# Optimization experiments

Measured on AMD Instinct MI355X. Metric: run time of the kernel, lower is better.

## Reference

```python
import jax, jax.numpy as jnp
import numpy as np

N, D = 8192, 1024
MAX_REP = 8

def setup_inputs() -> dict:
    key = jax.random.key(0)
    k1, k2 = jax.random.split(key)
    encoder_h = jax.random.normal(k1, (N, D), dtype=jnp.float32)
    repeats = jax.random.randint(k2, (N,), 0, MAX_REP, dtype=jnp.int32)
    return {"encoder_h": encoder_h, "repeats": repeats}

def reference(encoder_h, repeats):
    # Variable-length repeat_interleave along axis 0.
    # Equivalent to tf tile+sequence_mask+boolean_mask+reshape in the original,
    # but expressed as a single cumsum-index gather (no max_repeat-sized blowup).
    repeats = repeats.astype(jnp.int32)
    total = int(jnp.sum(repeats))  # dynamic output length (data-dependent)
    csum = jnp.cumsum(repeats)                     # [N]
    # row index for each output slot: searchsorted maps output position -> source row
    idx = jnp.searchsorted(csum, jnp.arange(total, dtype=jnp.int32), side='right')  # [total]
    return encoder_h[idx]                          # [total, D]
```

## Files before the change

### kernel.cpp

```cpp
#include <hip/hip_runtime.h>


#define SCAN_THREADS 1024
#define ELEMS_PER_THREAD 8

__global__ __launch_bounds__(SCAN_THREADS)
void scan_kernel(const int* __restrict__ repeats, int* __restrict__ csum, int n) {
    __shared__ int tmp[SCAN_THREADS];
    const int t = threadIdx.x;
    const int base = t * ELEMS_PER_THREAD;
    int vals[ELEMS_PER_THREAD];
    int s = 0;
#pragma unroll
    for (int j = 0; j < ELEMS_PER_THREAD; ++j) {
        const int idx = base + j;
        const int v = (idx < n) ? repeats[idx] : 0;
        vals[j] = v;
        s += v;
    }
    tmp[t] = s;
    __syncthreads();
    for (int off = 1; off < SCAN_THREADS; off <<= 1) {
        const int v = (t >= off) ? tmp[t - off] : 0;
        __syncthreads();
        tmp[t] += v;
        __syncthreads();
    }
    int run = tmp[t] - s;
#pragma unroll
    for (int j = 0; j < ELEMS_PER_THREAD; ++j) {
        run += vals[j];
        const int idx = base + j;
        if (idx < n) csum[idx] = run;
    }
}

__global__ __launch_bounds__(256)
void gather_rows_kernel(const float* __restrict__ h,
                        const int* __restrict__ csum,
                        float* __restrict__ out,
                        int n_rows_in, int d4 ) {
    const int row = blockIdx.x;
    int lo = 0, hi = n_rows_in;
    while (lo < hi) {
        const int mid = (lo + hi) >> 1;
        if (csum[mid] > row) hi = mid; else lo = mid + 1;
    }
    const float4* __restrict__ src = (const float4*)h + (size_t)lo * d4;
    float4* __restrict__ dst = (float4*)out + (size_t)row * d4;
    for (int i = threadIdx.x; i < d4; i += blockDim.x) {
        dst[i] = src[i];
    }
}

extern "C" void kernel_launch(void* const* d_in, const int* in_sizes, int n_in,
                              void* d_out, int out_size, void* d_ws, size_t ws_size,
                              hipStream_t stream) {
    const float* encoder_h = (const float*)d_in[0];
    const int*   repeats   = (const int*)d_in[1];
    float*       out       = (float*)d_out;

    const int n = in_sizes[1];
    const int d = in_sizes[0] / n;
    const int total_rows = out_size / d;

    int* csum = (int*)d_ws;

    scan_kernel<<<1, SCAN_THREADS, 0, stream>>>(repeats, csum, n);
    gather_rows_kernel<<<total_rows, 256, 0, stream>>>(encoder_h, csum, out,
                                                       n, d / 4);
}
```

Measured before the change: 170.6 us.

## Scatter explicit row index map in scan kernel; gather multiple rows per block

The scan kernel now writes each output row's source index directly into a workspace map, replacing the per-block binary search over the cumulative sum in the gather kernel. The gather kernel also handles four output rows per block, loading their indices up front. This removes about thirteen dependent global reads per output row before the copy starts and cuts block count. In exchange the single-block scan does serial scattered writes whose length varies per thread, and the workspace must hold total_rows ints instead of n.

```diff
diff --git a/kernel.cpp b/kernel.cpp
--- a/kernel.cpp
+++ b/kernel.cpp
@@ -3,9 +3,11 @@
 
 #define SCAN_THREADS 1024
 #define ELEMS_PER_THREAD 8
+#define ROWS_PER_BLOCK 4
 
 __global__ __launch_bounds__(SCAN_THREADS)
-void scan_kernel(const int* __restrict__ repeats, int* __restrict__ csum, int n) {
+void scan_scatter_kernel(const int* __restrict__ repeats,
+                         int* __restrict__ idx_map, int n) {
     __shared__ int tmp[SCAN_THREADS];
     const int t = threadIdx.x;
     const int base = t * ELEMS_PER_THREAD;
@@ -29,27 +31,36 @@
     int run = tmp[t] - s;
 #pragma unroll
     for (int j = 0; j < ELEMS_PER_THREAD; ++j) {
-        run += vals[j];
-        const int idx = base + j;
-        if (idx < n) csum[idx] = run;
+        const int src_row = base + j;
+        const int r = vals[j];
+        for (int k = 0; k < r; ++k) {
+            idx_map[run + k] = src_row;
+        }
+        run += r;
     }
 }
 
 __global__ __launch_bounds__(256)
-void gather_rows_kernel(const float* __restrict__ h,
-                        const int* __restrict__ csum,
-                        float* __restrict__ out,
-                        int n_rows_in, int d4 ) {
-    const int row = blockIdx.x;
-    int lo = 0, hi = n_rows_in;
-    while (lo < hi) {
-        const int mid = (lo + hi) >> 1;
-        if (csum[mid] > row) hi = mid; else lo = mid + 1;
+void gather_rows_kernel(const float4* __restrict__ h,
+                        const int* __restrict__ idx_map,
+                        float4* __restrict__ out,
+                        int total_rows, int d4 ) {
+    const int row0 = blockIdx.x * ROWS_PER_BLOCK;
+    int srcs[ROWS_PER_BLOCK];
+#pragma unroll
+    for (int r = 0; r < ROWS_PER_BLOCK; ++r) {
+        const int row = row0 + r;
+        srcs[r] = (row < total_rows) ? idx_map[row] : 0;
     }
-    const float4* __restrict__ src = (const float4*)h + (size_t)lo * d4;
-    float4* __restrict__ dst = (float4*)out + (size_t)row * d4;
-    for (int i = threadIdx.x; i < d4; i += blockDim.x) {
-        dst[i] = src[i];
+#pragma unroll
+    for (int r = 0; r < ROWS_PER_BLOCK; ++r) {
+        const int row = row0 + r;
+        if (row >= total_rows) return;
+        const float4* __restrict__ src = h + (size_t)srcs[r] * d4;
+        float4* __restrict__ dst = out + (size_t)row * d4;
+        for (int i = threadIdx.x; i < d4; i += blockDim.x) {
+            dst[i] = src[i];
+        }
     }
 }
 
@@ -64,9 +75,11 @@
     const int d = in_sizes[0] / n;
     const int total_rows = out_size / d;
 
-    int* csum = (int*)d_ws;
+    int* idx_map = (int*)d_ws;
 
-    scan_kernel<<<1, SCAN_THREADS, 0, stream>>>(repeats, csum, n);
-    gather_rows_kernel<<<total_rows, 256, 0, stream>>>(encoder_h, csum, out,
-                                                       n, d / 4);
+    scan_scatter_kernel<<<1, SCAN_THREADS, 0, stream>>>(repeats, idx_map, n);
+
+    const int nblocks = (total_rows + ROWS_PER_BLOCK - 1) / ROWS_PER_BLOCK;
+    gather_rows_kernel<<<nblocks, 256, 0, stream>>>(
+        (const float4*)encoder_h, idx_map, (float4*)out, total_rows, d / 4);
 }
```

Measured after the change: 160.9 us. 1.06x faster.

## Invert gather into per-source-row scatter and use wave-shuffle scan

Applied to the files above, without the earlier changes.

The gather kernel, which binary-searched the cumulative sum for every output row, is replaced by one block per input row. Each block reads its source row once and writes it r times, starting at an exclusive-prefix offset. The single-block scan now uses wavefront shuffles plus a serial pass over per-wave totals instead of a 1024-wide shared-memory Hillis-Steele loop. This removes the per-row binary search and the duplicate reads of repeated source rows, but the write work per block now varies with the repeat count (0 to 7).

```diff
diff --git a/kernel.cpp b/kernel.cpp
--- a/kernel.cpp
+++ b/kernel.cpp
@@ -1,14 +1,20 @@
 #include <hip/hip_runtime.h>
 
+
+typedef float nfloat4 __attribute__((ext_vector_type(4)));
 
 #define SCAN_THREADS 1024
 #define ELEMS_PER_THREAD 8
 
 __global__ __launch_bounds__(SCAN_THREADS)
-void scan_kernel(const int* __restrict__ repeats, int* __restrict__ csum, int n) {
-    __shared__ int tmp[SCAN_THREADS];
+void scan_kernel(const int* __restrict__ repeats,
+                 int* __restrict__ csum_excl, int n) {
+    __shared__ int wsum[SCAN_THREADS / 64];
     const int t = threadIdx.x;
+    const int lane = t & 63;
+    const int wave = t >> 6;
     const int base = t * ELEMS_PER_THREAD;
+
     int vals[ELEMS_PER_THREAD];
     int s = 0;
 #pragma unroll
@@ -18,38 +24,50 @@
         vals[j] = v;
         s += v;
     }
-    tmp[t] = s;
+    int isum = s;
+#pragma unroll
+    for (int off = 1; off < 64; off <<= 1) {
+        const int v = __shfl_up(isum, off, 64);
+        if (lane >= off) isum += v;
+    }
+    if (lane == 63) wsum[wave] = isum;
     __syncthreads();
-    for (int off = 1; off < SCAN_THREADS; off <<= 1) {
-        const int v = (t >= off) ? tmp[t - off] : 0;
-        __syncthreads();
-        tmp[t] += v;
-        __syncthreads();
+    if (t == 0) {
+        int acc = 0;
+#pragma unroll
+        for (int w = 0; w < SCAN_THREADS / 64; ++w) {
+            const int v = wsum[w];
+            wsum[w] = acc;
+            acc += v;
+        }
     }
-    int run = tmp[t] - s;
+    __syncthreads();
+    int run = wsum[wave] + isum - s;
 #pragma unroll
     for (int j = 0; j < ELEMS_PER_THREAD; ++j) {
+        const int idx = base + j;
+        if (idx < n) csum_excl[idx] = run;
         run += vals[j];
-        const int idx = base + j;
-        if (idx < n) csum[idx] = run;
     }
 }
 
 __global__ __launch_bounds__(256)
-void gather_rows_kernel(const float* __restrict__ h,
-                        const int* __restrict__ csum,
-                        float* __restrict__ out,
-                        int n_rows_in, int d4 ) {
+void spread_rows_kernel(const nfloat4* __restrict__ h,
+                        const int* __restrict__ repeats,
+                        const int* __restrict__ csum_excl,
+                        nfloat4* __restrict__ out,
+                        int d4 ) {
     const int row = blockIdx.x;
-    int lo = 0, hi = n_rows_in;
-    while (lo < hi) {
-        const int mid = (lo + hi) >> 1;
-        if (csum[mid] > row) hi = mid; else lo = mid + 1;
-    }
-    const float4* __restrict__ src = (const float4*)h + (size_t)lo * d4;
-    float4* __restrict__ dst = (float4*)out + (size_t)row * d4;
+    const int r = repeats[row];
+    if (r == 0) return;
+    const int obase = csum_excl[row];
+    const nfloat4* __restrict__ src = h + (size_t)row * d4;
+    nfloat4* __restrict__ dst0 = out + (size_t)obase * d4;
     for (int i = threadIdx.x; i < d4; i += blockDim.x) {
-        dst[i] = src[i];
+        const nfloat4 v = src[i];
+        for (int k = 0; k < r; ++k) {
+            dst0[(size_t)k * d4 + i] = v;
+        }
     }
 }
 
@@ -62,11 +80,10 @@
 
     const int n = in_sizes[1];
     const int d = in_sizes[0] / n;
-    const int total_rows = out_size / d;
 
-    int* csum = (int*)d_ws;
+    int* csum_excl = (int*)d_ws;
 
-    scan_kernel<<<1, SCAN_THREADS, 0, stream>>>(repeats, csum, n);
-    gather_rows_kernel<<<total_rows, 256, 0, stream>>>(encoder_h, csum, out,
-                                                       n, d / 4);
+    scan_kernel<<<1, SCAN_THREADS, 0, stream>>>(repeats, csum_excl, n);
+    spread_rows_kernel<<<n, 256, 0, stream>>>(
+        (const nfloat4*)encoder_h, repeats, csum_excl, (nfloat4*)out, d / 4);
 }
```

Result: faster. 155.3 us (-9.0%).
